# Optimization experiments

Measured on AMD Instinct MI355X. Metric: run time of the kernel, lower is better.

Reference implementation:

```python
import jax, jax.numpy as jnp
import numpy as np

B, N, C_IN, C_OUT, K, KS = 8, 2048, 64, 64, 20, 20


def _paiconv(x, feature, kernals, one_padding, mlp_w, mlp_b, conv_w, conv_b,
             mlp_out_w, mlp_out_b, bn_gamma, bn_beta):
    b, c, n = feature.shape
    pts = jnp.transpose(x, (0, 2, 1))                       # [B,N,3]
    sq = jnp.sum(pts * pts, axis=-1)                        # [B,N]
    d2 = sq[:, :, None] + sq[:, None, :] - 2.0 * jnp.einsum('bnd,bmd->bnm', pts, pts)
    _, idx = jax.lax.top_k(-d2, K)                          # [B,N,K] nearest (self first)
    bidx = jnp.arange(b)[:, None, None]
    x_neighs = pts[bidx, idx].reshape(b * n, K, 3)          # [BN,K,3]
    x_repeat = jnp.broadcast_to(x_neighs[:, :1, :], x_neighs.shape)
    x_rel = x_neighs - x_repeat                             # [BN,K,3]
    x_dis = jnp.sqrt(jnp.sum(x_rel * x_rel, axis=-1, keepdims=True) + 1e-12)
    x_feats7 = jnp.concatenate([x_repeat, x_rel, x_dis], axis=-1)  # [BN,K,7]
    # pointwise MLP (Conv1d 7->in_c, kernel 1)
    x_feats = jnp.einsum('nkc,oc->nok', x_feats7, mlp_w) + mlp_b[None, :, None]  # [BN,C,K]
    featsT = jnp.transpose(feature, (0, 2, 1))              # [B,N,C]
    neigh_feats = featsT[bidx, idx].reshape(b * n, K, c)    # [BN,K,C]
    feats = jnp.concatenate([jnp.transpose(neigh_feats, (0, 2, 1)), x_feats], axis=1)  # [BN,2C,K]
    # permutation matrix with threshold + double normalization (topkmax)
    perm = jnp.einsum('nkd,dm->nkm', x_rel, kernals) + one_padding  # [BN,K,KS]
    perm = jnp.where(perm > 0, perm, 0.0)
    perm = perm / (jnp.sum(perm, axis=1, keepdims=True) + 1e-6)
    perm = perm * perm
    perm = perm / (jnp.sum(perm, axis=1, keepdims=True) + 1e-6)
    perm = jnp.where(perm > 0.1, perm, 0.0)
    agg = jnp.einsum('nck,nkm->ncm', feats, perm).reshape(b * n, 2 * c * KS)
    out = (agg @ conv_w.T + conv_b).reshape(b, n, C_OUT)
    out = jnp.transpose(out, (0, 2, 1)) \
        + jnp.einsum('bcn,oc->bon', feature, mlp_out_w) + mlp_out_b[None, :, None]
    # BatchNorm1d (training-mode batch stats, biased variance, eps=1e-5)
    mean = jnp.mean(out, axis=(0, 2), keepdims=True)
    var = jnp.var(out, axis=(0, 2), keepdims=True)
    out = (out - mean) / jnp.sqrt(var + 1e-5)
    return out * bn_gamma[None, :, None] + bn_beta[None, :, None]


def setup_inputs() -> dict:
    key = jax.random.key(0)
    ks = jax.random.split(key, 10)
    one_padding = jnp.zeros((K, KS), jnp.float32).at[0, 0].set(1.0)
    return {
        'x': jax.random.normal(ks[0], (B, 3, N), jnp.float32),
        'feature': jax.random.normal(ks[1], (B, C_IN, N), jnp.float32),
        'kernals': jax.random.normal(ks[2], (3, KS), jnp.float32),
        'one_padding': one_padding,
        'mlp_w': jax.random.normal(ks[3], (C_IN, 7), jnp.float32) * 0.2,
        'mlp_b': jnp.zeros((C_IN,), jnp.float32),
        'conv_w': jax.random.normal(ks[4], (C_OUT, 2 * C_IN * KS), jnp.float32) * 0.02,
        'conv_b': jnp.zeros((C_OUT,), jnp.float32),
        'mlp_out_w': jax.random.normal(ks[5], (C_OUT, C_IN), jnp.float32) * 0.1,
        'mlp_out_b': jnp.zeros((C_OUT,), jnp.float32),
        'bn_gamma': jnp.ones((C_OUT,), jnp.float32),
        'bn_beta': jnp.zeros((C_OUT,), jnp.float32),
    }


def reference(x, feature, kernals, one_padding, mlp_w, mlp_b, conv_w, conv_b,
              mlp_out_w, mlp_out_b, bn_gamma, bn_beta):
    return _paiconv(x, feature, kernals, one_padding, mlp_w, mlp_b, conv_w, conv_b,
                    mlp_out_w, mlp_out_b, bn_gamma, bn_beta)
```

## Files before the change

### kernel.cpp

```cpp
#include <hip/hip_runtime.h>
#include <cstddef>

#define BB   8
#define NN   2048
#define CIN  64
#define COUT 64
#define KK   20
#define KSS  20
#define C2   128
#define PPB  4
#define NC   24
#define KT   80
#define AGG_LD 2576

typedef _Float16 h2t  __attribute__((ext_vector_type(2)));
typedef _Float16 f16x8 __attribute__((ext_vector_type(8)));
typedef float    f32x4 __attribute__((ext_vector_type(4)));

__device__ __forceinline__ unsigned pk2(float a, float b) {
    unsigned short ua = __builtin_bit_cast(unsigned short, (_Float16)a);
    unsigned short ub = __builtin_bit_cast(unsigned short, (_Float16)b);
    return (unsigned)ua | ((unsigned)ub << 16);
}

__device__ __forceinline__ unsigned wave_min_u32(unsigned v) {
    unsigned x = v, t;
    t = (unsigned)__builtin_amdgcn_update_dpp((int)x, (int)x, 0x111, 0xf, 0xf, false);
    x = (t < x) ? t : x;
    t = (unsigned)__builtin_amdgcn_update_dpp((int)x, (int)x, 0x112, 0xf, 0xf, false);
    x = (t < x) ? t : x;
    t = (unsigned)__builtin_amdgcn_update_dpp((int)x, (int)x, 0x114, 0xf, 0xf, false);
    x = (t < x) ? t : x;
    t = (unsigned)__builtin_amdgcn_update_dpp((int)x, (int)x, 0x118, 0xf, 0xf, false);
    x = (t < x) ? t : x;
    t = (unsigned)__builtin_amdgcn_update_dpp((int)x, (int)x, 0x142, 0xf, 0xf, false);
    x = (t < x) ? t : x;
    t = (unsigned)__builtin_amdgcn_update_dpp((int)x, (int)x, 0x143, 0xf, 0xf, false);
    x = (t < x) ? t : x;
    return (unsigned)__builtin_amdgcn_readlane((int)x, 63);
}

__global__ __launch_bounds__(256) void prep_kernel(
    const float* __restrict__ cw, const float* __restrict__ mw,
    uint4* __restrict__ aFrag, float* __restrict__ mowT)
{
    int i = blockIdx.x * 256 + threadIdx.x;
    if (i < 4 * KT * 64) {
        int wv = i / (KT * 64);
        int r  = i - wv * (KT * 64);
        int t  = r >> 6, l = r & 63;
        int o  = (wv << 4) + (l & 15);
        int j  = (t << 5) + ((l >> 4) << 3);
        const float* s = cw + (size_t)o * (C2 * KSS) + j;
        uint4 v;
        v.x = pk2(s[0], s[1]);
        v.y = pk2(s[2], s[3]);
        v.z = pk2(s[4], s[5]);
        v.w = pk2(s[6], s[7]);
        aFrag[i] = v;
    }
    if (i < COUT * CIN) {
        int o = i >> 6, c = i & 63;
        mowT[c * COUT + o] = mw[o * CIN + c];
    }
}

__global__ __launch_bounds__(256) void tr_kernel(
    const float* __restrict__ f, float* __restrict__ ft)
{
    __shared__ float tile[64][65];
    const int bt = blockIdx.x;
    const int b  = bt >> 5;
    const int n0 = (bt & 31) << 6;
    const int tn  = threadIdx.x & 63;
    const int tc0 = threadIdx.x >> 6;
#pragma unroll
    for (int r = 0; r < 16; ++r) {
        int c = (r << 2) + tc0;
        tile[c][tn] = f[((size_t)(b * CIN + c)) * NN + n0 + tn];
    }
    __syncthreads();
#pragma unroll
    for (int r = 0; r < 16; ++r) {
        int n = (r << 2) + tc0;
        ft[((size_t)b * NN + n0 + n) * CIN + tn] = tile[tn][n];
    }
}

__global__ __launch_bounds__(256, 4) void knn_kernel(
    const float* __restrict__ x, int* __restrict__ nid)
{
    const int tid  = threadIdx.x;
    const int w    = tid >> 6;
    const int lane = tid & 63;
    const int p    = blockIdx.x * 4 + w;
    const int b    = p >> 11;
    const int n    = p & (NN - 1);

    const float* xb0 = x + (size_t)(b * 3 + 0) * NN;
    const float* xb1 = x + (size_t)(b * 3 + 1) * NN;
    const float* xb2 = x + (size_t)(b * 3 + 2) * NN;

    const unsigned long long SENT = 0xFFFFFFFFFFFFFFFFull;
    const float qx = xb0[n], qy = xb1[n], qz = xb2[n];

    float d2r[32];
#pragma unroll
    for (int j = 0; j < 32; ++j) {
        int m = lane + 64 * j;
        float dx = xb0[m] - qx;
        float dy = xb1[m] - qy;
        float dz = xb2[m] - qz;
        d2r[j] = dx * dx + dy * dy + dz * dz;
    }

    unsigned long long c0 = SENT, c1 = SENT, c2 = SENT;
#pragma unroll
    for (int j = 0; j < 32; ++j) {
        unsigned long long pk =
            ((unsigned long long)__float_as_uint(d2r[j]) << 32)
            | (unsigned)(lane + 64 * j);
        if (pk < c0)      { c2 = c1; c1 = c0; c0 = pk; }
        else if (pk < c1) { c2 = c1; c1 = pk; }
        else if (pk < c2) { c2 = pk; }
    }

    unsigned killmask = 0u;
    unsigned long long mypk = SENT;
    for (int k = 0; k < NC; ++k) {
        unsigned myd  = (unsigned)(c0 >> 32);
        unsigned dmin = wave_min_u32(myd);
        unsigned idxc = (myd == dmin) ? (unsigned)c0 : 0xFFFFFFFFu;
        unsigned imin = wave_min_u32(idxc);
        unsigned long long bp = ((unsigned long long)dmin << 32) | imin;

        if (lane == k) mypk = bp;
        if (c0 == bp) {
            killmask |= 1u << ((unsigned)(bp & 0xFFFFFFFFull) >> 6);
            c0 = c1; c1 = c2; c2 = SENT;
            if (c0 == SENT) {
#pragma unroll
                for (int j = 0; j < 32; ++j) {
                    if (!(killmask & (1u << j))) {
                        unsigned long long pk =
                            ((unsigned long long)__float_as_uint(d2r[j]) << 32)
                            | (unsigned)(lane + 64 * j);
                        if (pk < c0)      { c2 = c1; c1 = c0; c0 = pk; }
                        else if (pk < c1) { c2 = c1; c1 = pk; }
                        else if (pk < c2) { c2 = pk; }
                    }
                }
            }
        }
    }

    double dd = 1e300;
    int ci = 0x7fffffff;
    if (lane < NC) {
        ci = (int)(mypk & 0xFFFFFFFFull);
        double dx = (double)xb0[ci] - (double)qx;
        double dy = (double)xb1[ci] - (double)qy;
        double dz = (double)xb2[ci] - (double)qz;
        dd = dx * dx + dy * dy + dz * dz;
    }
    unsigned long long db = __double_as_longlong(dd);
#pragma unroll
    for (int size = 2; size <= 32; size <<= 1) {
#pragma unroll
        for (int stride = size >> 1; stride > 0; stride >>= 1) {
            unsigned long long odb = __shfl_xor(db, stride);
            int oci = __shfl_xor(ci, stride);
            bool up = ((lane & size) == 0);
            bool takemin = (((lane & stride) == 0) == up);
            bool oless = (odb < db) || (odb == db && oci < ci);
            if (takemin == oless) { db = odb; ci = oci; }
        }
    }
    if (lane < KK) nid[(size_t)p * KK + lane] = ci;
}

__global__ __launch_bounds__(256, 3) void point_kernel(
    const float* __restrict__ x,
    const float* __restrict__ featT,
    const float* __restrict__ kern,
    const float* __restrict__ pad,
    const float* __restrict__ mlp_w,
    const float* __restrict__ mlp_b,
    const uint4* __restrict__ aFrag,
    const float* __restrict__ conv_b,
    const float* __restrict__ mowT,
    const float* __restrict__ mob,
    const int* __restrict__ nid,
    float* __restrict__ out)
{
    __shared__ __align__(16) _Float16 agg_h[PPB][AGG_LD];
    __shared__ __align__(16) float u_s[PPB * KK * KSS];
    __shared__ float xr_s[PPB][KK][3];
    __shared__ float xd_s[PPB][KK];
    __shared__ float xrep_s[PPB][3];
    __shared__ float colden_s[PPB][KSS];
    __shared__ float fcol_s[PPB][CIN];
    __shared__ int   nid_s[PPB][KK];

    float (*perm_s)[KK][KSS] = (float (*)[KK][KSS])u_s;
    float (*red2)[COUT]      = (float (*)[COUT])u_s;

    const int tid  = threadIdx.x;
    const int w    = tid >> 6;
    const int lane = tid & 63;
    const int p    = blockIdx.x * PPB + w;
    const int b    = p >> 11;
    const int n    = p & (NN - 1);

    const float* xb0 = x + (size_t)(b * 3 + 0) * NN;
    const float* xb1 = x + (size_t)(b * 3 + 1) * NN;
    const float* xb2 = x + (size_t)(b * 3 + 2) * NN;

    if (lane < KK) nid_s[w][lane] = nid[(size_t)p * KK + lane];

    fcol_s[w][lane] = featT[((size_t)b * NN + n) * CIN + lane];

    if (lane == 0) {
        int m0 = nid_s[w][0];
        xrep_s[w][0] = xb0[m0]; xrep_s[w][1] = xb1[m0]; xrep_s[w][2] = xb2[m0];
    }
    if (lane < KK) {
        int m = nid_s[w][lane];
        float rx = xb0[m] - xrep_s[w][0];
        float ry = xb1[m] - xrep_s[w][1];
        float rz = xb2[m] - xrep_s[w][2];
        xr_s[w][lane][0] = rx; xr_s[w][lane][1] = ry; xr_s[w][lane][2] = rz;
        xd_s[w][lane] = sqrtf(rx * rx + ry * ry + rz * rz + 1e-12f);
    }

    for (int e = lane; e < KK * KSS; e += 64) {
        int k = e / KSS, m = e % KSS;
        float v = xr_s[w][k][0] * kern[0 * KSS + m]
                + xr_s[w][k][1] * kern[1 * KSS + m]
                + xr_s[w][k][2] * kern[2 * KSS + m]
                + pad[k * KSS + m];
        perm_s[w][k][m] = v > 0.0f ? v : 0.0f;
    }
    if (lane < KSS) {
        float s = 0.0f;
        for (int k = 0; k < KK; ++k) s += perm_s[w][k][lane];
        colden_s[w][lane] = s + 1e-6f;
    }
    for (int e = lane; e < KK * KSS; e += 64) {
        int k = e / KSS, m = e % KSS;
        float v = perm_s[w][k][m] / colden_s[w][m];
        perm_s[w][k][m] = v * v;
    }
    if (lane < KSS) {
        float s = 0.0f;
        for (int k = 0; k < KK; ++k) s += perm_s[w][k][lane];
        colden_s[w][lane] = s + 1e-6f;
    }
    for (int e = lane; e < KK * KSS; e += 64) {
        int k = e / KSS, m = e % KSS;
        float v = perm_s[w][k][m] / colden_s[w][m];
        perm_s[w][k][m] = v > 0.1f ? v : 0.0f;
    }

    float fg[KK], fm[KK];
#pragma unroll
    for (int k = 0; k < KK; ++k)
        fg[k] = featT[((size_t)b * NN + nid_s[w][k]) * CIN + lane];
    {
        float w0 = mlp_w[lane * 7 + 0], w1 = mlp_w[lane * 7 + 1];
        float w2 = mlp_w[lane * 7 + 2], w3 = mlp_w[lane * 7 + 3];
        float w4 = mlp_w[lane * 7 + 4], w5 = mlp_w[lane * 7 + 5];
        float w6 = mlp_w[lane * 7 + 6];
        float bias = mlp_b[lane];
#pragma unroll
        for (int k = 0; k < KK; ++k) {
            fm[k] = xrep_s[w][0] * w0 + xrep_s[w][1] * w1 + xrep_s[w][2] * w2
                  + xr_s[w][k][0] * w3 + xr_s[w][k][1] * w4 + xr_s[w][k][2] * w5
                  + xd_s[w][k] * w6 + bias;
        }
    }

#pragma unroll
    for (int m4 = 0; m4 < KSS / 4; ++m4) {
        float sx = 0.f, sy = 0.f, sz = 0.f, sw = 0.f;
        float tx = 0.f, ty = 0.f, tz = 0.f, tw = 0.f;
#pragma unroll
        for (int k = 0; k < KK; ++k) {
            const float4 pv = *(const float4*)&perm_s[w][k][m4 * 4];
            const float a = fg[k], c = fm[k];
            sx += a * pv.x; sy += a * pv.y; sz += a * pv.z; sw += a * pv.w;
            tx += c * pv.x; ty += c * pv.y; tz += c * pv.z; tw += c * pv.w;
        }
        const int mb = m4 * 4;
        agg_h[w][lane * KSS + mb + 0]         = (_Float16)sx;
        agg_h[w][lane * KSS + mb + 1]         = (_Float16)sy;
        agg_h[w][lane * KSS + mb + 2]         = (_Float16)sz;
        agg_h[w][lane * KSS + mb + 3]         = (_Float16)sw;
        agg_h[w][(CIN + lane) * KSS + mb + 0] = (_Float16)tx;
        agg_h[w][(CIN + lane) * KSS + mb + 1] = (_Float16)ty;
        agg_h[w][(CIN + lane) * KSS + mb + 2] = (_Float16)tz;
        agg_h[w][(CIN + lane) * KSS + mb + 3] = (_Float16)tw;
    }
    __syncthreads();

    {
        f32x4 acc0 = {0.f, 0.f, 0.f, 0.f};
        f32x4 acc1 = {0.f, 0.f, 0.f, 0.f};
        const uint4* ap = aFrag + (size_t)(w * KT) * 64 + lane;
        const _Float16* bp = &agg_h[lane & 3][(lane >> 4) * 8];
#pragma unroll 4
        for (int t = 0; t < KT; t += 2) {
            uint4 av0 = ap[(size_t)t * 64];
            uint4 av1 = ap[(size_t)(t + 1) * 64];
            f16x8 b0 = *(const f16x8*)(bp + t * 32);
            f16x8 b1 = *(const f16x8*)(bp + (t + 1) * 32);
            acc0 = __builtin_amdgcn_mfma_f32_16x16x32_f16(
                       __builtin_bit_cast(f16x8, av0), b0, acc0, 0, 0, 0);
            acc1 = __builtin_amdgcn_mfma_f32_16x16x32_f16(
                       __builtin_bit_cast(f16x8, av1), b1, acc1, 0, 0, 0);
        }
        acc0 += acc1;
        if ((lane & 15) < 4) {
            const int p2 = lane & 15;
            const int ob = (w << 4) + ((lane >> 4) << 2);
            *(f32x4*)&red2[p2][ob] = acc0;
        }
    }
    __syncthreads();

    {
        float acc = conv_b[lane] + red2[w][lane];
        for (int c = 0; c < CIN; ++c)
            acc += fcol_s[w][c] * mowT[c * COUT + lane];
        acc += mob[lane];
        out[(size_t)(b * COUT + lane) * NN + n] = acc;
    }
}

__global__ __launch_bounds__(256) void bn_reduce(
    const float* __restrict__ out, float* __restrict__ part)
{
    const int o = blockIdx.x >> 3;
    const int s = blockIdx.x & 7;
    const float* src = out + (size_t)(s * COUT + o) * NN;
    float a = 0.f, q = 0.f;
    for (int i = threadIdx.x; i < NN; i += 256) {
        float v = src[i];
        a += v; q += v * v;
    }
    __shared__ float s1[256], s2[256];
    s1[threadIdx.x] = a; s2[threadIdx.x] = q;
    __syncthreads();
    for (int st = 128; st > 0; st >>= 1) {
        if (threadIdx.x < st) {
            s1[threadIdx.x] += s1[threadIdx.x + st];
            s2[threadIdx.x] += s2[threadIdx.x + st];
        }
        __syncthreads();
    }
    if (threadIdx.x == 0) {
        part[(o * 8 + s) * 2 + 0] = s1[0];
        part[(o * 8 + s) * 2 + 1] = s2[0];
    }
}

__global__ __launch_bounds__(256) void bn_apply(
    float* __restrict__ out, const float* __restrict__ part,
    const float* __restrict__ gamma, const float* __restrict__ beta)
{
    const int o = blockIdx.x >> 3;
    const int s = blockIdx.x & 7;
    float a = 0.f, q = 0.f;
#pragma unroll
    for (int t = 0; t < 8; ++t) {
        a += part[(o * 8 + t) * 2 + 0];
        q += part[(o * 8 + t) * 2 + 1];
    }
    const float M = (float)(BB * NN);
    const float mean = a / M;
    float var = q / M - mean * mean;
    if (var < 0.f) var = 0.f;
    const float inv = 1.0f / sqrtf(var + 1e-5f);
    const float g = gamma[o] * inv, be = beta[o];
    float* dst = out + (size_t)(s * COUT + o) * NN;
    for (int i = threadIdx.x; i < NN; i += 256) {
        dst[i] = (dst[i] - mean) * g + be;
    }
}

extern "C" void kernel_launch(void* const* d_in, const int* in_sizes, int n_in,
                              void* d_out, int out_size, void* d_ws, size_t ws_size,
                              hipStream_t stream)
{
    const float* x       = (const float*)d_in[0];
    const float* feature = (const float*)d_in[1];
    const float* kern    = (const float*)d_in[2];
    const float* pad     = (const float*)d_in[3];
    const float* mlp_w   = (const float*)d_in[4];
    const float* mlp_b   = (const float*)d_in[5];
    const float* conv_w  = (const float*)d_in[6];
    const float* conv_b  = (const float*)d_in[7];
    const float* mow     = (const float*)d_in[8];
    const float* mob     = (const float*)d_in[9];
    const float* gamma   = (const float*)d_in[10];
    const float* beta    = (const float*)d_in[11];

    char* wsp = (char*)d_ws;
    uint4* aFrag = (uint4*)wsp;
    float* mowT  = (float*)(wsp + 327680);
    float* part  = (float*)(wsp + 327680 + 16384);
    int*   nid   = (int*)(wsp + 327680 + 16384 + 4096);
    float* featT = (float*)(wsp + 327680 + 16384 + 4096 + 1310720);

    float* out = (float*)d_out;

    prep_kernel<<<(4 * KT * 64 + 255) / 256, 256, 0, stream>>>(conv_w, mow, aFrag, mowT);
    tr_kernel<<<BB * (NN / 64), 256, 0, stream>>>(feature, featT);
    knn_kernel<<<BB * NN / 4, 256, 0, stream>>>(x, nid);
    point_kernel<<<BB * NN / PPB, 256, 0, stream>>>(x, featT, kern, pad,
                                                    mlp_w, mlp_b, aFrag, conv_b,
                                                    mowT, mob, nid, out);
    bn_reduce<<<512, 256, 0, stream>>>(out, part);
    bn_apply<<<512, 256, 0, stream>>>(out, part, gamma, beta);
}
```

Before: 249.8 us.

## Recompute kNN distances instead of caching, vectorize loads and LDS stores

The kNN kernel stops keeping 32 per-lane distances in registers. It streams float4 point loads with FMA-based distance math and recomputes distances from global memory when a lane's candidate list runs dry, which allows raising the occupancy hint to 8 blocks. The killmask indexing is remapped to the new contiguous point assignment. Separately, the fused kernel packs fp16 aggregate stores into 64-bit LDS writes and reads the feature column via float4 in an unrolled output-MLP loop. The trade-off is extra global loads on refill, in exchange for lower register pressure. Because dx*dx etc. are now fused, distances may round slightly differently from the separate multiply-add form, which could change tie ordering in the candidate selection.

```diff
diff --git a/kernel.cpp b/kernel.cpp
--- a/kernel.cpp
+++ b/kernel.cpp
@@ -38,6 +38,12 @@
     t = (unsigned)__builtin_amdgcn_update_dpp((int)x, (int)x, 0x143, 0xf, 0xf, false);
     x = (t < x) ? t : x;
     return (unsigned)__builtin_amdgcn_readlane((int)x, 63);
+}
+
+__device__ __forceinline__ float d2f(float px, float py, float pz,
+                                     float qx, float qy, float qz) {
+    float dx = px - qx, dy = py - qy, dz = pz - qz;
+    return fmaf(dz, dz, fmaf(dy, dy, dx * dx));
 }
 
 __global__ __launch_bounds__(256) void prep_kernel(
@@ -87,7 +93,7 @@
     }
 }
 
-__global__ __launch_bounds__(256, 4) void knn_kernel(
+__global__ __launch_bounds__(256, 8) void knn_kernel(
     const float* __restrict__ x, int* __restrict__ nid)
 {
     const int tid  = threadIdx.x;
@@ -104,25 +110,26 @@
     const unsigned long long SENT = 0xFFFFFFFFFFFFFFFFull;
     const float qx = xb0[n], qy = xb1[n], qz = xb2[n];
 
-    float d2r[32];
-#pragma unroll
-    for (int j = 0; j < 32; ++j) {
-        int m = lane + 64 * j;
-        float dx = xb0[m] - qx;
-        float dy = xb1[m] - qy;
-        float dz = xb2[m] - qz;
-        d2r[j] = dx * dx + dy * dy + dz * dz;
-    }
-
     unsigned long long c0 = SENT, c1 = SENT, c2 = SENT;
 #pragma unroll
-    for (int j = 0; j < 32; ++j) {
-        unsigned long long pk =
-            ((unsigned long long)__float_as_uint(d2r[j]) << 32)
-            | (unsigned)(lane + 64 * j);
-        if (pk < c0)      { c2 = c1; c1 = c0; c0 = pk; }
-        else if (pk < c1) { c2 = c1; c1 = pk; }
-        else if (pk < c2) { c2 = pk; }
+    for (int jj = 0; jj < 8; ++jj) {
+        const int m0 = jj * 256 + lane * 4;
+        const float4 vx = *(const float4*)&xb0[m0];
+        const float4 vy = *(const float4*)&xb1[m0];
+        const float4 vz = *(const float4*)&xb2[m0];
+        const float dd4[4] = { d2f(vx.x, vy.x, vz.x, qx, qy, qz),
+                               d2f(vx.y, vy.y, vz.y, qx, qy, qz),
+                               d2f(vx.z, vy.z, vz.z, qx, qy, qz),
+                               d2f(vx.w, vy.w, vz.w, qx, qy, qz) };
+#pragma unroll
+        for (int e = 0; e < 4; ++e) {
+            unsigned long long pk =
+                ((unsigned long long)__float_as_uint(dd4[e]) << 32)
+                | (unsigned)(m0 + e);
+            if (pk < c0)      { c2 = c1; c1 = c0; c0 = pk; }
+            else if (pk < c1) { c2 = c1; c1 = pk; }
+            else if (pk < c2) { c2 = pk; }
+        }
     }
 
     unsigned killmask = 0u;
@@ -136,15 +143,25 @@
 
         if (lane == k) mypk = bp;
         if (c0 == bp) {
-            killmask |= 1u << ((unsigned)(bp & 0xFFFFFFFFull) >> 6);
+            unsigned mi = (unsigned)(bp & 0xFFFFFFFFull);
+            killmask |= 1u << (((mi >> 8) << 2) | (mi & 3));
             c0 = c1; c1 = c2; c2 = SENT;
             if (c0 == SENT) {
-#pragma unroll
-                for (int j = 0; j < 32; ++j) {
-                    if (!(killmask & (1u << j))) {
+                for (int jj = 0; jj < 8; ++jj) {
+                    const int m0 = jj * 256 + lane * 4;
+                    const float4 vx = *(const float4*)&xb0[m0];
+                    const float4 vy = *(const float4*)&xb1[m0];
+                    const float4 vz = *(const float4*)&xb2[m0];
+                    const float dd4[4] = { d2f(vx.x, vy.x, vz.x, qx, qy, qz),
+                                           d2f(vx.y, vy.y, vz.y, qx, qy, qz),
+                                           d2f(vx.z, vy.z, vz.z, qx, qy, qz),
+                                           d2f(vx.w, vy.w, vz.w, qx, qy, qz) };
+#pragma unroll
+                    for (int e = 0; e < 4; ++e) {
+                        if (killmask & (1u << ((jj << 2) | e))) continue;
                         unsigned long long pk =
-                            ((unsigned long long)__float_as_uint(d2r[j]) << 32)
-                            | (unsigned)(lane + 64 * j);
+                            ((unsigned long long)__float_as_uint(dd4[e]) << 32)
+                            | (unsigned)(m0 + e);
                         if (pk < c0)      { c2 = c1; c1 = c0; c0 = pk; }
                         else if (pk < c1) { c2 = c1; c1 = pk; }
                         else if (pk < c2) { c2 = pk; }
@@ -199,7 +216,7 @@
     __shared__ float xd_s[PPB][KK];
     __shared__ float xrep_s[PPB][3];
     __shared__ float colden_s[PPB][KSS];
-    __shared__ float fcol_s[PPB][CIN];
+    __shared__ __align__(16) float fcol_s[PPB][CIN];
     __shared__ int   nid_s[PPB][KK];
 
     float (*perm_s)[KK][KSS] = (float (*)[KK][KSS])u_s;
@@ -292,14 +309,10 @@
             tx += c * pv.x; ty += c * pv.y; tz += c * pv.z; tw += c * pv.w;
         }
         const int mb = m4 * 4;
-        agg_h[w][lane * KSS + mb + 0]         = (_Float16)sx;
-        agg_h[w][lane * KSS + mb + 1]         = (_Float16)sy;
-        agg_h[w][lane * KSS + mb + 2]         = (_Float16)sz;
-        agg_h[w][lane * KSS + mb + 3]         = (_Float16)sw;
-        agg_h[w][(CIN + lane) * KSS + mb + 0] = (_Float16)tx;
-        agg_h[w][(CIN + lane) * KSS + mb + 1] = (_Float16)ty;
-        agg_h[w][(CIN + lane) * KSS + mb + 2] = (_Float16)tz;
-        agg_h[w][(CIN + lane) * KSS + mb + 3] = (_Float16)tw;
+        uint2 ua; ua.x = pk2(sx, sy); ua.y = pk2(sz, sw);
+        *(uint2*)&agg_h[w][lane * KSS + mb] = ua;
+        uint2 ub; ub.x = pk2(tx, ty); ub.y = pk2(tz, tw);
+        *(uint2*)&agg_h[w][(CIN + lane) * KSS + mb] = ub;
     }
     __syncthreads();
 
@@ -330,8 +343,15 @@
 
     {
         float acc = conv_b[lane] + red2[w][lane];
-        for (int c = 0; c < CIN; ++c)
-            acc += fcol_s[w][c] * mowT[c * COUT + lane];
+        const float4* f4 = (const float4*)fcol_s[w];
+#pragma unroll
+        for (int c4 = 0; c4 < CIN / 4; ++c4) {
+            float4 fv = f4[c4];
+            acc += fv.x * mowT[(c4 * 4 + 0) * COUT + lane];
+            acc += fv.y * mowT[(c4 * 4 + 1) * COUT + lane];
+            acc += fv.z * mowT[(c4 * 4 + 2) * COUT + lane];
+            acc += fv.w * mowT[(c4 * 4 + 3) * COUT + lane];
+        }
         acc += mob[lane];
         out[(size_t)(b * COUT + lane) * NN + n] = acc;
     }
```

After: 290.6 us. +16.3%, slower.
